# Kernel tuning notes

Hardware: AMD Instinct MI355X
Metric: run time of the kernel (lower is better)

## Reference

```python
import jax, jax.numpy as jnp
import numpy as np

H, G, D = 16, 4, 64  # heads, n_global, head_dim
DM = H * D           # 1024 hidden size
B, N = 8, 4096


def setup_inputs() -> dict:
    key = jax.random.key(0)
    ks = jax.random.split(key, 16)
    std = 0.02
    def lin(k, fi, fo):
        return jax.random.normal(k, (fi, fo), dtype=jnp.float32) * std
    return {
        "hidden_states": jax.random.normal(ks[0], (B, N, DM), dtype=jnp.float32),
        "attention_mask": jnp.zeros((B, 1, N), dtype=jnp.float32),
        "Wq": lin(ks[1], DM, DM), "bq": jnp.zeros((DM,), jnp.float32),
        "Wqa": lin(ks[2], DM, H * G), "bqa": jnp.zeros((H * G,), jnp.float32),
        "Wk": lin(ks[3], DM, DM), "bk": jnp.zeros((DM,), jnp.float32),
        "Wka": lin(ks[4], DM, H * G), "bka": jnp.zeros((H * G,), jnp.float32),
        "Wv": lin(ks[5], DM, DM), "bv": jnp.zeros((DM,), jnp.float32),
        "Wt": lin(ks[6], DM, DM), "bt": jnp.zeros((DM,), jnp.float32),
    }


def reference(hidden_states, attention_mask, Wq, bq, Wqa, bqa, Wk, bk, Wka, bka, Wv, bv, Wt, bt):
    b, n, _ = hidden_states.shape
    scale = D ** 0.5
    q = hidden_states @ Wq + bq            # b n (h d)
    k = hidden_states @ Wk + bk
    v = hidden_states @ Wv + bv
    # query attention scores: b n (h g) -> b h g n
    qs = (q @ Wqa + bqa).reshape(b, n, H, G).transpose(0, 2, 3, 1) / scale
    qs = qs + attention_mask[:, None]      # broadcast over h (and g)
    qw = jax.nn.softmax(qs, axis=-1)       # b h g n
    mq = q.reshape(b, n, H, D).transpose(0, 2, 1, 3)   # b h n d
    gq = jnp.einsum('bhgn,bhnd->bhdg', qw, mq)          # b h d g
    kh = k.reshape(b, n, H, D).transpose(0, 2, 1, 3)    # b h n d
    qk = kh[..., None] * gq[:, :, None]                 # b h n d g
    qk = qk.transpose(0, 2, 1, 3, 4).reshape(b, n, H * D, G)
    qk = jnp.max(qk, axis=-1)                           # b n (h d)
    # NOTE: original code adds mask but does NOT softmax this score
    ksc = (qk @ Wka + bka).reshape(b, n, H, G).transpose(0, 2, 3, 1) / scale
    ksc = ksc + attention_mask[:, None]                 # b h g n
    gk = jnp.einsum('bhgn,bhnd->bhdg', ksc, kh)         # b h d g
    vh = v.reshape(b, n, H, D).transpose(0, 2, 1, 3)    # b h n d
    u = gk[:, :, None] * vh[..., None]                  # b h n d g
    u = jnp.max(u, axis=-1)                             # b h n d
    u = u.transpose(0, 2, 1, 3).reshape(b, n, H * D)    # b n (h d)
    r = u @ Wt + bt
    return r + q
```

## Files before the change

kernel.cpp:

```cpp
#include <hip/hip_runtime.h>
#include <hip/hip_bf16.h>

typedef __bf16 bf16;
typedef __attribute__((ext_vector_type(8))) __bf16 bf16x8;
typedef __attribute__((ext_vector_type(4))) float floatx4;


__device__ __forceinline__ void gload_lds16(const void* g, void* l) {
    __builtin_amdgcn_global_load_lds(
        (const __attribute__((address_space(1))) unsigned int*)g,
        (__attribute__((address_space(3))) unsigned int*)l, 16, 0, 0);
}

#define WAIT_LGKM0() asm volatile("s_waitcnt lgkmcnt(0)" ::: "memory")
#define WAIT_VM(N) asm volatile("s_waitcnt vmcnt(" #N ")" ::: "memory")

__global__ __launch_bounds__(256)
void cvt_kernel(const float* __restrict__ src, bf16* __restrict__ dst, int n8) {
    int i8 = blockIdx.x * 256 + threadIdx.x;
    if (i8 >= n8) return;
    const float* s = src + (size_t)i8 * 8;
    float4 x = *(const float4*)s;
    float4 y = *(const float4*)(s + 4);
    bf16x8 o;
    o[0] = (bf16)x.x; o[1] = (bf16)x.y; o[2] = (bf16)x.z; o[3] = (bf16)x.w;
    o[4] = (bf16)y.x; o[5] = (bf16)y.y; o[6] = (bf16)y.z; o[7] = (bf16)y.w;
    *(bf16x8*)(dst + (size_t)i8 * 8) = o;
}

__global__ __launch_bounds__(256)
void transpose_cvt_kernel(const float* __restrict__ src, bf16* __restrict__ dst, int R, int C) {
    __shared__ bf16 tile[64][65];
    int tr0 = blockIdx.x * 64;
    int tc0 = blockIdx.y * 64;
    int tx = threadIdx.x & 63, ty = threadIdx.x >> 6;
#pragma unroll
    for (int j = 0; j < 16; j++) {
        int r = ty + j * 4;
        tile[tx][r] = (bf16)src[(size_t)(tr0 + r) * C + tc0 + tx];
    }
    __syncthreads();
#pragma unroll
    for (int j = 0; j < 16; j++) {
        int r = ty + j * 4;
        dst[(size_t)(tc0 + r) * R + tr0 + tx] = tile[r][tx];
    }
}

__global__ __launch_bounds__(256)
void biaspack_kernel(const float* __restrict__ bq, const float* __restrict__ bk,
                     const float* __restrict__ bv, float* __restrict__ biasf,
                     float* __restrict__ zbias) {
    int i = blockIdx.x * 256 + threadIdx.x;
    if (i < 1024)      biasf[i] = bq[i];
    else if (i < 2048) biasf[i] = bk[i - 1024];
    else if (i < 3072) biasf[i] = bv[i - 2048];
    else if (i < 3200) biasf[i] = 0.f;
    else if (i < 4224) zbias[i - 3200] = 0.f;
}

__global__ __launch_bounds__(64)
void compbias_kernel(const float* __restrict__ bq, const float* __restrict__ Wqa,
                     const float* __restrict__ bqa, float* __restrict__ out) {
    int j = threadIdx.x;
    float a = 0.f;
    for (int t = 0; t < 1024; t++) a += bq[t] * Wqa[(size_t)t * 64 + j];
    out[j] = a + bqa[j];
}

template<int BN, int WN, int EPI>
__global__ __launch_bounds__(WN * 128)
void gemm_kernel(const bf16* __restrict__ A, int lda,
                 const bf16* __restrict__ WT,
                 const float* __restrict__ bias,
                 void* __restrict__ Cout, int ldc,
                 const float* __restrict__ mask,
                 const bf16* __restrict__ qadd, int ldq,
                 int K) {
    constexpr int BM = 128;
    constexpr int NT = WN * 128;
    __shared__ bf16 As[BM * 32];
    __shared__ bf16 Bs[BN * 32];

    const int tid  = threadIdx.x;
    const int wid  = tid >> 6;
    const int lane = tid & 63;
    const int l16  = lane & 15;
    const int quad = lane >> 4;
    const int wm   = wid & 1;
    const int wn   = wid >> 1;
    const int m0   = blockIdx.x * BM;
    const int n0   = blockIdx.y * BN;

    floatx4 acc[4][4];
#pragma unroll
    for (int i = 0; i < 4; i++)
#pragma unroll
        for (int j = 0; j < 4; j++) acc[i][j] = (floatx4)0.0f;

    for (int k0 = 0; k0 < K; k0 += 32) {
        __syncthreads();
#pragma unroll
        for (int i = tid; i < BM * 4; i += NT) {
            const bf16* gp = A + (size_t)(m0 + (i >> 2)) * lda + k0 + (i & 3) * 8;
            gload_lds16(gp, (char*)As + (size_t)(i & ~63) * 16);
        }
#pragma unroll
        for (int i = tid; i < BN * 4; i += NT) {
            const bf16* gp = WT + (size_t)(n0 + (i >> 2)) * K + k0 + (i & 3) * 8;
            gload_lds16(gp, (char*)Bs + (size_t)(i & ~63) * 16);
        }
        __syncthreads();
        bf16x8 af[4], bfv[4];
#pragma unroll
        for (int mi = 0; mi < 4; mi++)
            af[mi] = *(const bf16x8*)&As[(wm * 64 + mi * 16 + l16) * 32 + quad * 8];
#pragma unroll
        for (int ni = 0; ni < 4; ni++)
            bfv[ni] = *(const bf16x8*)&Bs[(wn * 64 + ni * 16 + l16) * 32 + quad * 8];
#pragma unroll
        for (int mi = 0; mi < 4; mi++)
#pragma unroll
            for (int ni = 0; ni < 4; ni++)
                acc[mi][ni] = __builtin_amdgcn_mfma_f32_16x16x32_bf16(
                    af[mi], bfv[ni], acc[mi][ni], 0, 0, 0);
    }

#pragma unroll
    for (int mi = 0; mi < 4; mi++) {
#pragma unroll
        for (int ni = 0; ni < 4; ni++) {
            int col  = n0 + wn * 64 + ni * 16 + l16;
            int rowb = m0 + wm * 64 + mi * 16 + quad * 4;
            float bv = bias[col];
#pragma unroll
            for (int e = 0; e < 4; e++) {
                int row = rowb + e;
                float v = acc[mi][ni][e] + bv;
                if (EPI == 0) {
                    ((bf16*)Cout)[(size_t)row * ldc + col] = (bf16)v;
                } else if (EPI == 2) {
                    ((float*)Cout)[(size_t)row * ldc + col] = v * 0.125f + mask[row];
                } else {
                    v += (float)qadd[(size_t)row * ldq + col];
                    ((float*)Cout)[(size_t)row * ldc + col] = v;
                }
            }
        }
    }
}

#define DO_MFMA(MH, NH)                                                              \
    _Pragma("unroll")                                                                \
    for (int r_ = 0; r_ < 4; ++r_) {                                                 \
        _Pragma("unroll")                                                            \
        for (int nj_ = 0; nj_ < 2; ++nj_) {                                          \
            _Pragma("unroll")                                                        \
            for (int kk_ = 0; kk_ < 2; ++kk_) {                                      \
                acc[(MH) * 4 + r_][(NH) * 2 + nj_] =                                 \
                    __builtin_amdgcn_mfma_f32_16x16x32_bf16(                         \
                        af[r_][kk_], bfv[(NH) * 2 + nj_][kk_],                       \
                        acc[(MH) * 4 + r_][(NH) * 2 + nj_], 0, 0, 0);                \
            }                                                                        \
        }                                                                            \
    }

#define LOAD_A(MQ, BS)                                                               \
    _Pragma("unroll")                                                                \
    for (int r_ = 0; r_ < 4; ++r_)                                                   \
        _Pragma("unroll")                                                            \
        for (int kk_ = 0; kk_ < 2; ++kk_)                                            \
            af[r_][kk_] = *(const bf16x8*)(lA + (BS) + (MQ) * 8192 + r_ * 2048 + kk_ * 1024);

#define LOAD_B(NQ, BS)                                                               \
    _Pragma("unroll")                                                                \
    for (int nj_ = 0; nj_ < 2; ++nj_)                                                \
        _Pragma("unroll")                                                            \
        for (int kk_ = 0; kk_ < 2; ++kk_)                                            \
            bfv[(NQ) * 2 + nj_][kk_] =                                               \
                *(const bf16x8*)(lB + (BS) + (NQ) * 4096 + nj_ * 2048 + kk_ * 1024);

#define STAGE_A(H, KT, P) do {                                                       \
    gload_lds16(gA##H##0 + (KT) * 128, smem + (P) * 32768 + (H) * 16384 + ldsc);     \
    gload_lds16(gA##H##1 + (KT) * 128, smem + (P) * 32768 + (H) * 16384 + 8192 + ldsc); \
} while (0)

#define STAGE_B(H, KT, P) do {                                                       \
    gload_lds16(gB##H##0 + (KT) * 128, smem + 65536 + (P) * 32768 + (H) * 16384 + ldsc); \
    gload_lds16(gB##H##1 + (KT) * 128, smem + 65536 + (P) * 32768 + (H) * 16384 + 8192 + ldsc); \
} while (0)

template<int EPI, int NTILES>
__global__ __launch_bounds__(512, 2)
void gemm256_kernel(const bf16* __restrict__ A, int lda,
                    const bf16* __restrict__ B, int ldb,
                    const float* __restrict__ bias,
                    void* __restrict__ Cout, int ldc, int ncols,
                    const bf16* __restrict__ qadd, int ldq,
                    int ntn) {
    extern __shared__ __align__(16) char smem[];
    const int tid  = threadIdx.x;
    const int wid  = tid >> 6;
    const int lane = tid & 63;
    const int l16  = lane & 15;
    const int quad = lane >> 4;
    const int wm   = wid >> 2;
    const int wn   = wid & 3;

    const int nwg  = gridDim.x * gridDim.y;
    const int orig = blockIdx.y * gridDim.x + blockIdx.x;
    int swz = orig;
    if ((nwg & 7) == 0) swz = (orig & 7) * (nwg >> 3) + (orig >> 3);
    const int m0 = (swz / ntn) * 256;
    const int n0 = (swz % ntn) * 256;

    const int w2   = wid >> 1;
    const int cg   = wid & 1;
    const int lrow = lane >> 2;
    const int lcb8 = ((lane & 3) ^ ((lane >> 5) << 1)) << 3;
    const int ldsc = w2 * 2048 + cg * 1024;
    const int aoff = (l16 * 64 + quad * 16) ^ ((l16 & 8) << 2);

    const char* gA00 = (const char*)A + ((size_t)(m0 + w2 * 16 + lrow) * lda + (cg << 5) + lcb8) * 2;
    const char* gA01 = gA00 + (size_t)64 * lda * 2;
    const char* gA10 = gA00 + (size_t)128 * lda * 2;
    const char* gA11 = gA00 + (size_t)192 * lda * 2;
    const char* gB00 = (const char*)B + ((size_t)(n0 + w2 * 16 + lrow) * ldb + (cg << 5) + lcb8) * 2;
    const char* gB01 = gB00 + (size_t)64 * ldb * 2;
    const char* gB10 = gB00 + (size_t)128 * ldb * 2;
    const char* gB11 = gB00 + (size_t)192 * ldb * 2;

    const char* lA = smem + wm * 16384 + aoff;
    const char* lB = smem + 65536 + wn * 8192 + aoff;

    floatx4 acc[8][4];
#pragma unroll
    for (int i = 0; i < 8; ++i)
#pragma unroll
        for (int j = 0; j < 4; ++j) acc[i][j] = (floatx4)0.0f;

    STAGE_B(0, 0, 0);
    STAGE_B(1, 0, 0);
    STAGE_A(0, 0, 0);
    STAGE_A(1, 0, 0);
    STAGE_B(0, 1, 1);
    STAGE_B(1, 1, 1);
    WAIT_VM(4);
    __builtin_amdgcn_s_barrier();

#pragma unroll
    for (int t = 0; t < NTILES; ++t) {
        bf16x8 af[4][2], bfv[4][2];

        LOAD_A(0, (t & 1) * 32768)
        LOAD_B(0, (t & 1) * 32768)
        if (t + 1 < NTILES) STAGE_A(0, t + 1, (t + 1) & 1);
        __builtin_amdgcn_s_barrier();
        WAIT_LGKM0();
        __builtin_amdgcn_s_setprio(1);
        DO_MFMA(0, 0)
        __builtin_amdgcn_s_setprio(0);
        __builtin_amdgcn_s_barrier();

        LOAD_B(1, (t & 1) * 32768)
        if (t + 1 < NTILES) STAGE_A(1, t + 1, (t + 1) & 1);
        __builtin_amdgcn_s_barrier();
        WAIT_LGKM0();
        __builtin_amdgcn_s_setprio(1);
        DO_MFMA(0, 1)
        __builtin_amdgcn_s_setprio(0);
        __builtin_amdgcn_s_barrier();

        LOAD_A(1, (t & 1) * 32768)
        if (t + 2 < NTILES) STAGE_B(0, t + 2, t & 1);
        __builtin_amdgcn_s_barrier();
        WAIT_LGKM0();
        __builtin_amdgcn_s_setprio(1);
        DO_MFMA(1, 0)
        __builtin_amdgcn_s_setprio(0);
        __builtin_amdgcn_s_barrier();

        if (t + 2 < NTILES) STAGE_B(1, t + 2, t & 1);
        __builtin_amdgcn_s_barrier();
        __builtin_amdgcn_s_setprio(1);
        DO_MFMA(1, 1)
        __builtin_amdgcn_s_setprio(0);
        if (t < NTILES - 2) {
            WAIT_VM(4);
            __builtin_amdgcn_s_barrier();
        } else if (t == NTILES - 2) {
            WAIT_VM(0);
            __builtin_amdgcn_s_barrier();
        }
    }

#pragma unroll
    for (int mi = 0; mi < 8; ++mi) {
#pragma unroll
        for (int ni = 0; ni < 4; ++ni) {
            int col  = n0 + wn * 64 + ni * 16 + l16;
            int rowb = m0 + wm * 128 + mi * 16 + quad * 4;
            if (col < ncols) {
                float bv = bias[col];
#pragma unroll
                for (int e = 0; e < 4; ++e) {
                    int row = rowb + e;
                    float v = acc[mi][ni][e] + bv;
                    if (EPI == 0) {
                        ((bf16*)Cout)[(size_t)row * ldc + col] = (bf16)v;
                    } else {
                        v += (float)qadd[(size_t)row * ldq + col];
                        ((float*)Cout)[(size_t)row * ldc + col] = v;
                    }
                }
            }
        }
    }
}

__global__ __launch_bounds__(256)
void softmax_kernel(const bf16* __restrict__ qkv, const float* __restrict__ mask,
                    float* __restrict__ qw) {
    int bh = blockIdx.x;
    int b = bh >> 6, hg = bh & 63;
    int tid = threadIdx.x;
    float xs[16];
    float mx = -1e30f;
#pragma unroll
    for (int j = 0; j < 16; j++) {
        int n = tid + j * 256;
        float x = (float)qkv[(size_t)(b * 4096 + n) * 3200 + 3072 + hg] * 0.125f
                  + mask[b * 4096 + n];
        xs[j] = x;
        mx = fmaxf(mx, x);
    }
    __shared__ float red[256];
    red[tid] = mx;
    __syncthreads();
    for (int s = 128; s > 0; s >>= 1) {
        if (tid < s) red[tid] = fmaxf(red[tid], red[tid + s]);
        __syncthreads();
    }
    mx = red[0];
    __syncthreads();
    float sum = 0.f;
#pragma unroll
    for (int j = 0; j < 16; j++) { xs[j] = __expf(xs[j] - mx); sum += xs[j]; }
    red[tid] = sum;
    __syncthreads();
    for (int s = 128; s > 0; s >>= 1) {
        if (tid < s) red[tid] += red[tid + s];
        __syncthreads();
    }
    float inv = 1.0f / red[0];
#pragma unroll
    for (int j = 0; j < 16; j++)
        qw[(size_t)bh * 4096 + tid + j * 256] = xs[j] * inv;
}

__global__ __launch_bounds__(256)
void gq1_kernel(const float* __restrict__ qw, const bf16* __restrict__ qkv,
                float* __restrict__ part) {
    int bh = blockIdx.x, ch = blockIdx.y;
    int b = bh >> 4, h = bh & 15;
    int tid = threadIdx.x;
    int g = tid >> 6, d = tid & 63;
    const float* wrow = qw + ((size_t)(b * 64 + h * 4 + g)) * 4096 + ch * 256;
    const bf16* qcol  = qkv + (size_t)(b * 4096 + ch * 256) * 3200 + h * 64 + d;
    float a = 0.f;
#pragma unroll 8
    for (int n = 0; n < 256; n++)
        a += wrow[n] * (float)qcol[(size_t)n * 3200];
    part[(((size_t)bh * 16 + ch) * 4 + g) * 64 + d] = a;
}

__global__ __launch_bounds__(256)
void gk1_kernel(const float* __restrict__ ksc, const bf16* __restrict__ qkv,
                float* __restrict__ part) {
    int bh = blockIdx.x, ch = blockIdx.y;
    int b = bh >> 4, h = bh & 15;
    int tid = threadIdx.x;
    int g = tid >> 6, d = tid & 63;
    const float* sbase = ksc + (size_t)(b * 4096 + ch * 256) * 64 + h * 4 + g;
    const bf16* kcol   = qkv + (size_t)(b * 4096 + ch * 256) * 3200 + 1024 + h * 64 + d;
    float a = 0.f;
#pragma unroll 8
    for (int n = 0; n < 256; n++)
        a += sbase[(size_t)n * 64] * (float)kcol[(size_t)n * 3200];
    part[(((size_t)bh * 16 + ch) * 4 + g) * 64 + d] = a;
}

__global__ __launch_bounds__(256)
void gred_kernel(const float* __restrict__ part,
                 float* __restrict__ gmax, float* __restrict__ gmin) {
    int bh = blockIdx.x;
    int tid = threadIdx.x;
    int g = tid >> 6, d = tid & 63;
    float a = 0.f;
#pragma unroll
    for (int c = 0; c < 16; c++)
        a += part[(((size_t)bh * 16 + c) * 4 + g) * 64 + d];
    __shared__ float sg[4][64];
    sg[g][d] = a;
    __syncthreads();
    if (tid < 64) {
        float mx = sg[0][tid], mn = sg[0][tid];
#pragma unroll
        for (int gg = 1; gg < 4; gg++) {
            mx = fmaxf(mx, sg[gg][tid]);
            mn = fminf(mn, sg[gg][tid]);
        }
        gmax[bh * 64 + tid] = mx;
        gmin[bh * 64 + tid] = mn;
    }
}

__global__ __launch_bounds__(256)
void maxg_kernel(const bf16* __restrict__ qkv, int coloff,
                 const float* __restrict__ gmax, const float* __restrict__ gmin,
                 bf16* __restrict__ dst) {
    size_t i8 = (size_t)blockIdx.x * 256 + threadIdx.x;
    size_t e0 = i8 * 8;
    int row = (int)(e0 >> 10);
    int c   = (int)(e0 & 1023);
    int b   = row >> 12;
    bf16x8 kv = *(const bf16x8*)(qkv + (size_t)row * 3200 + coloff + c);
    bf16x8 out;
#pragma unroll
    for (int j = 0; j < 8; j++) {
        float f  = (float)kv[j];
        float gm = gmax[b * 1024 + c + j];
        float gn = gmin[b * 1024 + c + j];
        out[j] = (bf16)(f >= 0.f ? f * gm : f * gn);
    }
    *(bf16x8*)(dst + e0) = out;
}

extern "C" void kernel_launch(void* const* d_in, const int* in_sizes, int n_in,
                              void* d_out, int out_size, void* d_ws, size_t ws_size,
                              hipStream_t stream) {
    const float* hs   = (const float*)d_in[0];
    const float* mask = (const float*)d_in[1];
    const float* Wq   = (const float*)d_in[2];
    const float* bq   = (const float*)d_in[3];
    const float* Wqa  = (const float*)d_in[4];
    const float* bqa  = (const float*)d_in[5];
    const float* Wk   = (const float*)d_in[6];
    const float* bk   = (const float*)d_in[7];
    const float* Wka  = (const float*)d_in[8];
    const float* bka  = (const float*)d_in[9];
    const float* Wv   = (const float*)d_in[10];
    const float* bv   = (const float*)d_in[11];
    const float* Wt   = (const float*)d_in[12];
    const float* bt   = (const float*)d_in[13];

    char* p = (char*)d_ws;
    auto alloc = [&](size_t bytes) {
        char* r = p;
        p += (bytes + 255) & ~(size_t)255;
        return (void*)r;
    };
    bf16*  WT    = (bf16*) alloc((size_t)3328 * 1024 * 2);
    bf16*  WqBf  = (bf16*) alloc((size_t)1024 * 1024 * 2);
    bf16*  WqaT  = (bf16*) alloc((size_t)128 * 1024 * 2);
    bf16*  WkaT  = (bf16*) alloc((size_t)64 * 1024 * 2);
    bf16*  WtT   = (bf16*) alloc((size_t)1024 * 1024 * 2);
    float* biasf = (float*)alloc((size_t)3200 * 4);
    float* zbias = (float*)alloc((size_t)1024 * 4);
    bf16*  qkv   = (bf16*) alloc((size_t)32768 * 3200 * 2);
    bf16*  hsb   = (bf16*) alloc((size_t)32768 * 1024 * 2);
    float* qw    = (float*)alloc((size_t)512 * 4096 * 4);
    float* part  = (float*)alloc((size_t)128 * 16 * 256 * 4);
    float* gqmax = (float*)alloc((size_t)8192 * 4);
    float* gqmin = (float*)alloc((size_t)8192 * 4);
    float* gkmax = (float*)alloc((size_t)8192 * 4);
    float* gkmin = (float*)alloc((size_t)8192 * 4);
    bf16*  qk_u  = hsb;
    float* ksc   = qw;

    (void)hipFuncSetAttribute(reinterpret_cast<const void*>(&gemm256_kernel<0, 16>),
                              hipFuncAttributeMaxDynamicSharedMemorySize, 131072);
    (void)hipFuncSetAttribute(reinterpret_cast<const void*>(&gemm256_kernel<3, 16>),
                              hipFuncAttributeMaxDynamicSharedMemorySize, 131072);

    cvt_kernel<<<16384, 256, 0, stream>>>(hs, hsb, 4194304);
    cvt_kernel<<<512, 256, 0, stream>>>(Wq, WqBf, 131072);
    transpose_cvt_kernel<<<dim3(16, 16), 256, 0, stream>>>(Wq, WT, 1024, 1024);
    transpose_cvt_kernel<<<dim3(16, 16), 256, 0, stream>>>(Wk, WT + (size_t)1024 * 1024, 1024, 1024);
    transpose_cvt_kernel<<<dim3(16, 16), 256, 0, stream>>>(Wv, WT + (size_t)2048 * 1024, 1024, 1024);
    transpose_cvt_kernel<<<dim3(16, 1), 256, 0, stream>>>(Wqa, WqaT, 1024, 64);
    transpose_cvt_kernel<<<dim3(16, 1), 256, 0, stream>>>(Wka, WkaT, 1024, 64);
    transpose_cvt_kernel<<<dim3(16, 16), 256, 0, stream>>>(Wt, WtT, 1024, 1024);
    biaspack_kernel<<<17, 256, 0, stream>>>(bq, bk, bv, biasf, zbias);
    compbias_kernel<<<1, 64, 0, stream>>>(bq, Wqa, bqa, biasf + 3072);
    gemm_kernel<128, 2, 0><<<dim3(1, 8), 256, 0, stream>>>(
        WqaT, 1024, WqBf, zbias, WT + (size_t)3072 * 1024, 1024, nullptr, nullptr, 0, 1024);

    gemm256_kernel<0, 16><<<dim3(128, 13), 512, 131072, stream>>>(
        hsb, 1024, WT, 1024, biasf, qkv, 3200, 3200, nullptr, 0, 13);
    softmax_kernel<<<512, 256, 0, stream>>>(qkv, mask, qw);
    gq1_kernel<<<dim3(128, 16), 256, 0, stream>>>(qw, qkv, part);
    gred_kernel<<<128, 256, 0, stream>>>(part, gqmax, gqmin);
    maxg_kernel<<<16384, 256, 0, stream>>>(qkv, 1024, gqmax, gqmin, qk_u);
    gemm_kernel<64, 1, 2><<<dim3(256, 1), 128, 0, stream>>>(
        qk_u, 1024, WkaT, bka, ksc, 64, mask, nullptr, 0, 1024);
    gk1_kernel<<<dim3(128, 16), 256, 0, stream>>>(ksc, qkv, part);
    gred_kernel<<<128, 256, 0, stream>>>(part, gkmax, gkmin);
    maxg_kernel<<<16384, 256, 0, stream>>>(qkv, 2048, gkmax, gkmin, qk_u);
    gemm256_kernel<3, 16><<<dim3(128, 4), 512, 131072, stream>>>(
        qk_u, 1024, WtT, 1024, bt, d_out, 1024, 1024, qkv, 3200, 4);
}
```

Measured before the change: 912.2 us.

## Fuse max-of-global expansion into ksc GEMM and emit transposed query scores

A new GEMM kernel applies the per-channel max/min scaling of the key projection while loading its A tile. This removes the first maxg pass and its round trip through a bf16 buffer. The big QKV GEMM epilogue also writes scaled, masked query-attention logits in a transposed [b*hg, n] float layout, so the softmax reads contiguous rows instead of strided bf16 columns. The cost is extra scattered stores in the GEMM epilogue and a simple unpipelined loader in the new kernel.

New measurement: 883.7 us. 1.03x faster.

```diff
diff --git a/kernel.cpp b/kernel.cpp
--- a/kernel.cpp
+++ b/kernel.cpp
@@ -150,6 +150,90 @@
     }
 }
 
+__global__ __launch_bounds__(128)
+void gemmksc_kernel(const bf16* __restrict__ qkv,
+                    const bf16* __restrict__ WT,
+                    const float* __restrict__ bias,
+                    float* __restrict__ Cout,
+                    const float* __restrict__ mask,
+                    const float* __restrict__ gmax,
+                    const float* __restrict__ gmin) {
+    constexpr int BM = 128, BN = 64;
+    __shared__ bf16 As[BM * 32];
+    __shared__ bf16 Bs[BN * 32];
+    const int tid  = threadIdx.x;
+    const int wid  = tid >> 6;
+    const int lane = tid & 63;
+    const int l16  = lane & 15;
+    const int quad = lane >> 4;
+    const int wm   = wid & 1;
+    const int m0   = blockIdx.x * BM;
+    const int bb   = m0 >> 12;
+
+    floatx4 acc[4][4];
+#pragma unroll
+    for (int i = 0; i < 4; i++)
+#pragma unroll
+        for (int j = 0; j < 4; j++) acc[i][j] = (floatx4)0.0f;
+
+    for (int k0 = 0; k0 < 1024; k0 += 32) {
+        __syncthreads();
+#pragma unroll
+        for (int i = tid; i < BM * 4; i += 128) {
+            int row = m0 + (i >> 2);
+            int col = k0 + (i & 3) * 8;
+            bf16x8 kv = *(const bf16x8*)(qkv + (size_t)row * 3200 + 1024 + col);
+            float4 gm0 = *(const float4*)(gmax + bb * 1024 + col);
+            float4 gm1 = *(const float4*)(gmax + bb * 1024 + col + 4);
+            float4 gn0 = *(const float4*)(gmin + bb * 1024 + col);
+            float4 gn1 = *(const float4*)(gmin + bb * 1024 + col + 4);
+            float gms[8] = {gm0.x, gm0.y, gm0.z, gm0.w, gm1.x, gm1.y, gm1.z, gm1.w};
+            float gns[8] = {gn0.x, gn0.y, gn0.z, gn0.w, gn1.x, gn1.y, gn1.z, gn1.w};
+            bf16x8 o;
+#pragma unroll
+            for (int j = 0; j < 8; ++j) {
+                float f = (float)kv[j];
+                o[j] = (bf16)(f >= 0.f ? f * gms[j] : f * gns[j]);
+            }
+            *(bf16x8*)((char*)As + (size_t)i * 16) = o;
+        }
+#pragma unroll
+        for (int i = tid; i < BN * 4; i += 128) {
+            const bf16* gp = WT + (size_t)(i >> 2) * 1024 + k0 + (i & 3) * 8;
+            gload_lds16(gp, (char*)Bs + (size_t)(i & ~63) * 16);
+        }
+        __syncthreads();
+        bf16x8 af[4], bfv[4];
+#pragma unroll
+        for (int mi = 0; mi < 4; mi++)
+            af[mi] = *(const bf16x8*)&As[(wm * 64 + mi * 16 + l16) * 32 + quad * 8];
+#pragma unroll
+        for (int ni = 0; ni < 4; ni++)
+            bfv[ni] = *(const bf16x8*)&Bs[(ni * 16 + l16) * 32 + quad * 8];
+#pragma unroll
+        for (int mi = 0; mi < 4; mi++)
+#pragma unroll
+            for (int ni = 0; ni < 4; ni++)
+                acc[mi][ni] = __builtin_amdgcn_mfma_f32_16x16x32_bf16(
+                    af[mi], bfv[ni], acc[mi][ni], 0, 0, 0);
+    }
+
+#pragma unroll
+    for (int mi = 0; mi < 4; mi++) {
+#pragma unroll
+        for (int ni = 0; ni < 4; ni++) {
+            int col  = ni * 16 + l16;
+            int rowb = m0 + wm * 64 + mi * 16 + quad * 4;
+            float bv = bias[col];
+#pragma unroll
+            for (int e = 0; e < 4; e++) {
+                int row = rowb + e;
+                Cout[(size_t)row * 64 + col] = (acc[mi][ni][e] + bv) * 0.125f + mask[row];
+            }
+        }
+    }
+}
+
 #define DO_MFMA(MH, NH)                                                              \
     _Pragma("unroll")                                                                \
     for (int r_ = 0; r_ < 4; ++r_) {                                                 \
@@ -190,14 +274,17 @@
     gload_lds16(gB##H##1 + (KT) * 128, smem + 65536 + (P) * 32768 + (H) * 16384 + 8192 + ldsc); \
 } while (0)
 
-template<int EPI, int NTILES>
+template<int EPI, int QA>
 __global__ __launch_bounds__(512, 2)
 void gemm256_kernel(const bf16* __restrict__ A, int lda,
                     const bf16* __restrict__ B, int ldb,
                     const float* __restrict__ bias,
                     void* __restrict__ Cout, int ldc, int ncols,
                     const bf16* __restrict__ qadd, int ldq,
-                    int ntn) {
+                    int ntn,
+                    const float* __restrict__ mask,
+                    float* __restrict__ qaT) {
+    constexpr int NTILES = 16;
     extern __shared__ __align__(16) char smem[];
     const int tid  = threadIdx.x;
     const int wid  = tid >> 6;
@@ -308,6 +395,12 @@
                     float v = acc[mi][ni][e] + bv;
                     if (EPI == 0) {
                         ((bf16*)Cout)[(size_t)row * ldc + col] = (bf16)v;
+                        if (QA) {
+                            if (col >= 3072 && col < 3136) {
+                                qaT[(size_t)((row >> 12) * 64 + (col - 3072)) * 4096
+                                    + (row & 4095)] = v * 0.125f + mask[row];
+                            }
+                        }
                     } else {
                         v += (float)qadd[(size_t)row * ldq + col];
                         ((float*)Cout)[(size_t)row * ldc + col] = v;
@@ -319,18 +412,15 @@
 }
 
 __global__ __launch_bounds__(256)
-void softmax_kernel(const bf16* __restrict__ qkv, const float* __restrict__ mask,
-                    float* __restrict__ qw) {
+void softmax_kernel(const float* __restrict__ qaT, float* __restrict__ qw) {
     int bh = blockIdx.x;
-    int b = bh >> 6, hg = bh & 63;
     int tid = threadIdx.x;
+    const float* rowp = qaT + (size_t)bh * 4096;
     float xs[16];
     float mx = -1e30f;
 #pragma unroll
     for (int j = 0; j < 16; j++) {
-        int n = tid + j * 256;
-        float x = (float)qkv[(size_t)(b * 4096 + n) * 3200 + 3072 + hg] * 0.125f
-                  + mask[b * 4096 + n];
+        float x = rowp[tid + j * 256];
         xs[j] = x;
         mx = fmaxf(mx, x);
     }
@@ -476,11 +566,12 @@
     float* gkmax = (float*)alloc((size_t)8192 * 4);
     float* gkmin = (float*)alloc((size_t)8192 * 4);
     bf16*  qk_u  = hsb;
+    float* qaT   = qw;
     float* ksc   = qw;
 
-    (void)hipFuncSetAttribute(reinterpret_cast<const void*>(&gemm256_kernel<0, 16>),
+    (void)hipFuncSetAttribute(reinterpret_cast<const void*>(&gemm256_kernel<0, 1>),
                               hipFuncAttributeMaxDynamicSharedMemorySize, 131072);
-    (void)hipFuncSetAttribute(reinterpret_cast<const void*>(&gemm256_kernel<3, 16>),
+    (void)hipFuncSetAttribute(reinterpret_cast<const void*>(&gemm256_kernel<3, 0>),
                               hipFuncAttributeMaxDynamicSharedMemorySize, 131072);
 
     cvt_kernel<<<16384, 256, 0, stream>>>(hs, hsb, 4194304);
@@ -496,17 +587,15 @@
     gemm_kernel<128, 2, 0><<<dim3(1, 8), 256, 0, stream>>>(
         WqaT, 1024, WqBf, zbias, WT + (size_t)3072 * 1024, 1024, nullptr, nullptr, 0, 1024);
 
-    gemm256_kernel<0, 16><<<dim3(128, 13), 512, 131072, stream>>>(
-        hsb, 1024, WT, 1024, biasf, qkv, 3200, 3200, nullptr, 0, 13);
-    softmax_kernel<<<512, 256, 0, stream>>>(qkv, mask, qw);
+    gemm256_kernel<0, 1><<<dim3(128, 13), 512, 131072, stream>>>(
+        hsb, 1024, WT, 1024, biasf, qkv, 3200, 3200, nullptr, 0, 13, mask, qaT);
+    softmax_kernel<<<512, 256, 0, stream>>>(qaT, qw);
     gq1_kernel<<<dim3(128, 16), 256, 0, stream>>>(qw, qkv, part);
     gred_kernel<<<128, 256, 0, stream>>>(part, gqmax, gqmin);
-    maxg_kernel<<<16384, 256, 0, stream>>>(qkv, 1024, gqmax, gqmin, qk_u);
-    gemm_kernel<64, 1, 2><<<dim3(256, 1), 128, 0, stream>>>(
-        qk_u, 1024, WkaT, bka, ksc, 64, mask, nullptr, 0, 1024);
+    gemmksc_kernel<<<256, 128, 0, stream>>>(qkv, WkaT, bka, ksc, mask, gqmax, gqmin);
     gk1_kernel<<<dim3(128, 16), 256, 0, stream>>>(ksc, qkv, part);
     gred_kernel<<<128, 256, 0, stream>>>(part, gkmax, gkmin);
     maxg_kernel<<<16384, 256, 0, stream>>>(qkv, 2048, gkmax, gkmin, qk_u);
-    gemm256_kernel<3, 16><<<dim3(128, 4), 512, 131072, stream>>>(
-        qk_u, 1024, WtT, 1024, bt, d_out, 1024, 1024, qkv, 3200, 4);
-}
+    gemm256_kernel<3, 0><<<dim3(128, 4), 512, 131072, stream>>>(
+        qk_u, 1024, WtT, 1024, bt, d_out, 1024, 1024, qkv, 3200, 4, nullptr, nullptr);
+}
```
